# Performance work log

Hardware: AMD Instinct MI355X
Metric: run time of the kernel (lower is better)

## Reference

```python
import jax, jax.numpy as jnp
import numpy as np

HIDDEN = 4096
N_HEADS = 32
N_KV_HEADS = 8
HEAD_DIM = HIDDEN // N_HEADS  # 128
ROPE_THETA = 10000.0


def rotate_half(x):
    x1, x2 = jnp.split(x, 2, axis=-1)
    return jnp.concatenate((-x2, x1), axis=-1)


def rope_cos_sin(seq_len, dim, theta, dtype):
    inv_freq = 1.0 / (theta ** (jnp.arange(0, dim, 2, dtype=jnp.float32) / dim))
    t = jnp.arange(seq_len, dtype=jnp.float32)
    freqs = jnp.outer(t, inv_freq)               # [S, D/2]
    emb = jnp.concatenate((freqs, freqs), axis=-1)  # [S, D]
    return jnp.cos(emb).astype(dtype), jnp.sin(emb).astype(dtype)


def setup_inputs() -> dict:
    key = jax.random.key(0)
    k0, k1, k2, k3, k4 = jax.random.split(key, 5)
    B, S = 1, 2048
    std = 1.0 / np.sqrt(HIDDEN)
    return {
        "hidden_states": jax.random.normal(k0, (B, S, HIDDEN), dtype=jnp.float32),
        "wq": jax.random.normal(k1, (N_HEADS * HEAD_DIM, HIDDEN), dtype=jnp.float32) * std,
        "wk": jax.random.normal(k2, (N_KV_HEADS * HEAD_DIM, HIDDEN), dtype=jnp.float32) * std,
        "wv": jax.random.normal(k3, (N_KV_HEADS * HEAD_DIM, HIDDEN), dtype=jnp.float32) * std,
        "wo": jax.random.normal(k4, (HIDDEN, N_HEADS * HEAD_DIM), dtype=jnp.float32) * std,
    }


def reference(hidden_states, wq, wk, wv, wo):
    B, S, _ = hidden_states.shape
    dtype = hidden_states.dtype
    G = N_HEADS // N_KV_HEADS  # query groups per kv head

    # projections (torch Linear: x @ W.T)
    q = (hidden_states @ wq.T).reshape(B, S, N_HEADS, HEAD_DIM).transpose(0, 2, 1, 3)      # [B,H,S,D]
    k = (hidden_states @ wk.T).reshape(B, S, N_KV_HEADS, HEAD_DIM).transpose(0, 2, 1, 3)   # [B,Hkv,S,D]
    v = (hidden_states @ wv.T).reshape(B, S, N_KV_HEADS, HEAD_DIM).transpose(0, 2, 1, 3)   # [B,Hkv,S,D]

    cos, sin = rope_cos_sin(S, HEAD_DIM, ROPE_THETA, dtype)  # [S,D]
    cos = cos[None, None]  # [1,1,S,D]
    sin = sin[None, None]
    q = q * cos + rotate_half(q) * sin
    k = k * cos + rotate_half(k) * sin

    # GQA: group query heads with their kv head (equivalent to repeat_interleave on kv)
    qg = q.reshape(B, N_KV_HEADS, G, S, HEAD_DIM)
    scale = 1.0 / np.sqrt(HEAD_DIM)
    scores = jnp.einsum("bkgsd,bktd->bkgst", qg, k) * scale  # [B,Hkv,G,S,S]

    causal = jnp.tril(jnp.ones((S, S), dtype=bool))
    scores = jnp.where(causal, scores, -jnp.inf)
    probs = jax.nn.softmax(scores.astype(jnp.float32), axis=-1).astype(dtype)

    out = jnp.einsum("bkgst,bktd->bkgsd", probs, v)  # [B,Hkv,G,S,D]
    out = out.reshape(B, N_HEADS, S, HEAD_DIM).transpose(0, 2, 1, 3).reshape(B, S, N_HEADS * HEAD_DIM)
    return out @ wo.T
```

## Files before the change

kernel.cpp:

```cpp
#include <hip/hip_runtime.h>
#include <hip/hip_bf16.h>


typedef _Float16 half4_t __attribute__((ext_vector_type(4)));
typedef _Float16 half8_t __attribute__((ext_vector_type(8)));
typedef float f32x4 __attribute__((ext_vector_type(4)));

#define S_LEN 2048
#define HID 4096
#define NH 32
#define NKV 8

__device__ __forceinline__ void gload_lds16(const void* g, void* l) {
  __builtin_amdgcn_global_load_lds((const __attribute__((address_space(1))) void*)g,
                                   (__attribute__((address_space(3))) void*)l, 16, 0, 0);
}

__global__ __launch_bounds__(256) void cvt_f32_f16(const float* __restrict__ src,
                                                   _Float16* __restrict__ dst, int n4) {
  int i = blockIdx.x * 256 + threadIdx.x;
  if (i >= n4) return;
  f32x4 v = *(const f32x4*)(src + (size_t)i * 4);
  half4_t h = {(_Float16)v[0], (_Float16)v[1], (_Float16)v[2], (_Float16)v[3]};
  *(half4_t*)(dst + (size_t)i * 4) = h;
}

__global__ __launch_bounds__(256) void rope_table_kernel(float* __restrict__ cost,
                                                         float* __restrict__ sint) {
  int i = blockIdx.x * 256 + threadIdx.x;
  int d = i & 63;
  int s = i >> 6;
  float inv = exp2f(-(float)d * (13.287712379549449f / 64.0f));
  float f = (float)s * inv;
  cost[i] = cosf(f);
  sint[i] = sinf(f);
}

__global__ __launch_bounds__(256) void rope_apply_q(_Float16* __restrict__ X,
                                                    const float* __restrict__ cost,
                                                    const float* __restrict__ sint) {
  int idx = blockIdx.x * 256 + threadIdx.x;
  int g = idx & 15;
  int tmp = idx >> 4;
  int h = tmp % NH;
  int s = tmp / NH;
  int d0 = g * 4;
  size_t base = (size_t)s * HID + h * 128 + d0;
  half4_t x1 = *(half4_t*)(X + base);
  half4_t x2 = *(half4_t*)(X + base + 64);
  const float* cp = cost + s * 64 + d0;
  const float* sp = sint + s * 64 + d0;
  half4_t y1, y2;
#pragma unroll
  for (int j = 0; j < 4; ++j) {
    float c = cp[j], sn = sp[j];
    float a = (float)x1[j], b = (float)x2[j];
    y1[j] = (_Float16)(a * c - b * sn);
    y2[j] = (_Float16)(b * c + a * sn);
  }
  *(half4_t*)(X + base) = y1;
  *(half4_t*)(X + base + 64) = y2;
}

__global__ __launch_bounds__(256) void rope_k2_inplace(_Float16* __restrict__ K2,
                                                       const float* __restrict__ cost,
                                                       const float* __restrict__ sint) {
  int idx = blockIdx.x * 256 + threadIdx.x;
  int g = idx & 15;
  int tmp = idx >> 4;
  int h = tmp % NKV;
  int s = tmp / NKV;
  int d0 = g * 4;
  size_t tb = (size_t)h * (S_LEN * 128) + (size_t)(s >> 4) * 2048 + (size_t)(s & 15) * 8;
  size_t a1 = tb + (size_t)(d0 >> 3) * 128 + (d0 & 7);
  size_t a2 = a1 + 1024;
  half4_t x1 = *(half4_t*)(K2 + a1);
  half4_t x2 = *(half4_t*)(K2 + a2);
  const float* cp = cost + s * 64 + d0;
  const float* sp = sint + s * 64 + d0;
  half4_t y1, y2;
#pragma unroll
  for (int j = 0; j < 4; ++j) {
    float c = cp[j], sn = sp[j];
    float a = (float)x1[j], b = (float)x2[j];
    y1[j] = (_Float16)(a * c - b * sn);
    y2[j] = (_Float16)(b * c + a * sn);
  }
  *(half4_t*)(K2 + a1) = y1;
  *(half4_t*)(K2 + a2) = y2;
}

template <int MODE>
__global__ __launch_bounds__(256) void gemmC(const _Float16* __restrict__ A,
                                             const float* __restrict__ W0,
                                             const float* __restrict__ W1,
                                             const float* __restrict__ W2,
                                             void* __restrict__ out,
                                             _Float16* __restrict__ K2,
                                             _Float16* __restrict__ V2) {
  __shared__ __align__(16) _Float16 As[2][128 * 32];
  __shared__ __align__(16) _Float16 Bs[2][128 * 32];
  const int t = threadIdx.x, w = t >> 6, l = t & 63, lr = l & 15, lg = l >> 4;
  const int m0 = blockIdx.y * 128;
  const int bx = blockIdx.x;
  const float* Wp;
  int col0, sel;
  if (MODE == 1) {
    Wp = W0; col0 = bx * 128; sel = 0;
  } else {
    if (bx < 32)      { Wp = W0; col0 = bx * 128; sel = 0; }
    else if (bx < 40) { Wp = W1; col0 = (bx - 32) * 128; sel = 1; }
    else              { Wp = W2; col0 = (bx - 40) * 128; sel = 2; }
  }
  const int wm = (w >> 1) * 64, wn = (w & 1) * 64;
  const int srowA = l >> 2, scolA = (l & 3) * 8;
  const int srowB = t >> 2, scolB = (t & 3) * 8;
  const _Float16* ap = A + (size_t)m0 * 4096 + scolA;
  const float* bp = Wp + (size_t)col0 * 4096 + scolB;

  f32x4 acc[4][4] = {};
  f32x4 br[2][2];

#define GLOAD_A(buf_, kb_)                                            \
  _Pragma("unroll") for (int it = 0; it < 2; ++it) {                  \
    const int ci = it * 4 + w;                                        \
    const int r = ci * 16 + srowA;                                    \
    gload_lds16(ap + (size_t)r * 4096 + (kb_), &As[buf_][ci * 512]);  \
  }
#define LOAD_B(kb_)                                                   \
  _Pragma("unroll") for (int it = 0; it < 2; ++it) {                  \
    const float* p = bp + (size_t)(it * 64 + srowB) * 4096 + (kb_);   \
    br[it][0] = *(const f32x4*)p;                                     \
    br[it][1] = *(const f32x4*)(p + 4);                               \
  }
#define WRITE_B(buf_)                                                 \
  _Pragma("unroll") for (int it = 0; it < 2; ++it) {                  \
    half8_t hv;                                                       \
    _Pragma("unroll") for (int j = 0; j < 4; ++j) {                   \
      hv[j] = (_Float16)br[it][0][j];                                 \
      hv[4 + j] = (_Float16)br[it][1][j];                             \
    }                                                                 \
    *(half8_t*)&Bs[buf_][(it * 64 + srowB) * 32 + scolB] = hv;        \
  }

  LOAD_B(0)
  GLOAD_A(0, 0)
  WRITE_B(0)
  LOAD_B(32)
  __syncthreads();

  int cur = 0;
  for (int kb = 0; kb < 4096; kb += 32) {
    if (kb + 32 < 4096) {
      WRITE_B(cur ^ 1)
      GLOAD_A(cur ^ 1, kb + 32)
      if (kb + 64 < 4096) LOAD_B(kb + 64)
    }
    half8_t af[4], bf[4];
#pragma unroll
    for (int mi = 0; mi < 4; ++mi)
      af[mi] = *(const half8_t*)&As[cur][(wm + mi * 16 + lr) * 32 + lg * 8];
#pragma unroll
    for (int ni = 0; ni < 4; ++ni)
      bf[ni] = *(const half8_t*)&Bs[cur][(wn + ni * 16 + lr) * 32 + lg * 8];
#pragma unroll
    for (int mi = 0; mi < 4; ++mi)
#pragma unroll
      for (int ni = 0; ni < 4; ++ni)
        acc[mi][ni] = __builtin_amdgcn_mfma_f32_16x16x32_f16(af[mi], bf[ni], acc[mi][ni], 0, 0, 0);
    __syncthreads();
    cur ^= 1;
  }
#undef GLOAD_A
#undef LOAD_B
#undef WRITE_B

#pragma unroll
  for (int mi = 0; mi < 4; ++mi) {
#pragma unroll
    for (int ni = 0; ni < 4; ++ni) {
      const int row = m0 + wm + mi * 16 + lg * 4;
      const int col = col0 + wn + ni * 16 + lr;
      if (MODE == 1) {
#pragma unroll
        for (int i = 0; i < 4; ++i)
          ((float*)out)[(size_t)(row + i) * 4096 + col] = acc[mi][ni][i];
      } else if (sel == 0) {
#pragma unroll
        for (int i = 0; i < 4; ++i)
          ((_Float16*)out)[(size_t)(row + i) * 4096 + col] = (_Float16)acc[mi][ni][i];
      } else if (sel == 1) {
        const int h = col >> 7, d = col & 127;
        const size_t kb2 = (size_t)h * (S_LEN * 128) + (size_t)(row >> 4) * 2048 +
                           (size_t)(d >> 3) * 128 + (d & 7);
#pragma unroll
        for (int i = 0; i < 4; ++i)
          K2[kb2 + ((row + i) & 15) * 8] = (_Float16)acc[mi][ni][i];
      } else {
        half4_t o;
#pragma unroll
        for (int i = 0; i < 4; ++i) o[i] = (_Float16)acc[mi][ni][i];
        *(half4_t*)(V2 + (size_t)(col >> 7) * (S_LEN * 128) + (size_t)(row >> 4) * 2048 +
                    (size_t)(col & 127) * 16 + (row & 15)) = o;
      }
    }
  }
}

__global__ __launch_bounds__(256) void attn_kernel(const _Float16* __restrict__ Q,
                                                   const _Float16* __restrict__ K2,
                                                   const _Float16* __restrict__ V2,
                                                   _Float16* __restrict__ Op,
                                                   float* __restrict__ Md) {
  const int bid = blockIdx.x;
  const int hk = bid & 7;
  const int split = (bid >> 3) & 1;
  const int qt = 63 - (bid >> 4);
  const int w = threadIdx.x >> 6;
  const int h = hk * 4 + w;
  const int l = threadIdx.x & 63;
  const int lr = l & 15;
  const int lg = l >> 4;
  const float scale = 0.08838834764831845f;
  const float LOG2E = 1.4426950408889634f;
  const float NEG = -1.0e30f;

  const int half_steps = qt + 1;
  const int kt0 = split * half_steps;
  const int kt1 = kt0 + half_steps;

  int sq[2];
  half8_t qf[2][4];
#pragma unroll
  for (int qc = 0; qc < 2; ++qc) {
    sq[qc] = qt * 32 + qc * 16 + lr;
#pragma unroll
    for (int c = 0; c < 4; ++c)
      qf[qc][c] = *(const half8_t*)(Q + (size_t)sq[qc] * HID + h * 128 + c * 32 + lg * 8);
  }
  const _Float16* Kb = K2 + (size_t)hk * (S_LEN * 128);
  const _Float16* Vb = V2 + (size_t)hk * (S_LEN * 128);

  f32x4 acc[8][2] = {};
  float m[2] = {NEG, NEG};
  float den[2] = {0.f, 0.f};

  for (int kt = kt0; kt < kt1; ++kt) {
    half8_t kf[4];
#pragma unroll
    for (int c = 0; c < 4; ++c)
      kf[c] = *(const half8_t*)(Kb + (size_t)kt * 2048 + (c * 4 + lg) * 128 + lr * 8);
    f32x4 s0 = {0.f, 0.f, 0.f, 0.f}, s1 = {0.f, 0.f, 0.f, 0.f};
#pragma unroll
    for (int c = 0; c < 4; ++c) {
      s0 = __builtin_amdgcn_mfma_f32_16x16x32_f16(kf[c], qf[0][c], s0, 0, 0, 0);
      s1 = __builtin_amdgcn_mfma_f32_16x16x32_f16(kf[c], qf[1][c], s1, 0, 0, 0);
    }
    const int kbase = kt * 16 + lg * 4;
    float sc[2][4];
#pragma unroll
    for (int i = 0; i < 4; ++i) {
      sc[0][i] = s0[i] * scale;
      sc[1][i] = s1[i] * scale;
    }
    if (kt >= 2 * qt) {
#pragma unroll
      for (int qc = 0; qc < 2; ++qc)
#pragma unroll
        for (int i = 0; i < 4; ++i)
          if (kbase + i > sq[qc]) sc[qc][i] = NEG;
    }
    half4_t pf[2];
#pragma unroll
    for (int qc = 0; qc < 2; ++qc) {
      float mx = fmaxf(fmaxf(sc[qc][0], sc[qc][1]), fmaxf(sc[qc][2], sc[qc][3]));
      mx = fmaxf(mx, __shfl_xor(mx, 16));
      mx = fmaxf(mx, __shfl_xor(mx, 32));
      if (!__all(mx - m[qc] <= 8.0f)) {
        float mn = fmaxf(m[qc], mx);
        float corr = exp2f((m[qc] - mn) * LOG2E);
        den[qc] *= corr;
#pragma unroll
        for (int dc = 0; dc < 8; ++dc)
#pragma unroll
          for (int i = 0; i < 4; ++i) acc[dc][qc][i] *= corr;
        m[qc] = mn;
      }
      float ps = 0.f, p[4];
#pragma unroll
      for (int i = 0; i < 4; ++i) {
        p[i] = exp2f((sc[qc][i] - m[qc]) * LOG2E);
        ps += p[i];
      }
      ps += __shfl_xor(ps, 16);
      ps += __shfl_xor(ps, 32);
      den[qc] += ps;
      pf[qc] = (half4_t){(_Float16)p[0], (_Float16)p[1], (_Float16)p[2], (_Float16)p[3]};
    }
#pragma unroll
    for (int dc = 0; dc < 8; ++dc) {
      half4_t vf = *(const half4_t*)(Vb + (size_t)kt * 2048 + (dc * 16 + lr) * 16 + lg * 4);
      acc[dc][0] = __builtin_amdgcn_mfma_f32_16x16x16f16(vf, pf[0], acc[dc][0], 0, 0, 0);
      acc[dc][1] = __builtin_amdgcn_mfma_f32_16x16x16f16(vf, pf[1], acc[dc][1], 0, 0, 0);
    }
  }

  _Float16* Os = Op + (size_t)split * S_LEN * HID;
#pragma unroll
  for (int qc = 0; qc < 2; ++qc) {
    float inv = den[qc] > 0.f ? 1.0f / den[qc] : 0.f;
#pragma unroll
    for (int dc = 0; dc < 8; ++dc) {
      half4_t o;
#pragma unroll
      for (int i = 0; i < 4; ++i) o[i] = (_Float16)(acc[dc][qc][i] * inv);
      *(half4_t*)(Os + (size_t)sq[qc] * HID + h * 128 + dc * 16 + lg * 4) = o;
    }
    if (lg == 0) {
      int mdix = ((split * S_LEN + sq[qc]) * NH + h) * 2;
      Md[mdix] = m[qc];
      Md[mdix + 1] = den[qc];
    }
  }
}

__global__ __launch_bounds__(256) void attn_combine(const _Float16* __restrict__ Op,
                                                    const float* __restrict__ Md,
                                                    _Float16* __restrict__ O) {
  const float LOG2E = 1.4426950408889634f;
  int idx = blockIdx.x * 256 + threadIdx.x;
  int dd = (idx & 15) * 8;
  int h = (idx >> 4) & 31;
  int s = idx >> 9;
  int base = (s * NH + h) * 2;
  float m0 = Md[base], den0 = Md[base + 1];
  float m1 = Md[S_LEN * NH * 2 + base], den1 = Md[S_LEN * NH * 2 + base + 1];
  float M = fmaxf(m0, m1);
  float w0 = den0 * exp2f((m0 - M) * LOG2E);
  float w1 = den1 * exp2f((m1 - M) * LOG2E);
  float r = 1.0f / (w0 + w1);
  w0 *= r;
  w1 *= r;
  size_t off = (size_t)s * HID + h * 128 + dd;
  half8_t a = *(const half8_t*)(Op + off);
  half8_t b = *(const half8_t*)(Op + (size_t)S_LEN * HID + off);
  half8_t o;
#pragma unroll
  for (int j = 0; j < 8; ++j) o[j] = (_Float16)(w0 * (float)a[j] + w1 * (float)b[j]);
  *(half8_t*)(O + off) = o;
}

extern "C" void kernel_launch(void* const* d_in, const int* in_sizes, int n_in,
                              void* d_out, int out_size, void* d_ws, size_t ws_size,
                              hipStream_t stream) {
  (void)in_sizes; (void)n_in; (void)out_size; (void)ws_size;
  const float* hs = (const float*)d_in[0];
  const float* wq = (const float*)d_in[1];
  const float* wk = (const float*)d_in[2];
  const float* wv = (const float*)d_in[3];
  const float* wo = (const float*)d_in[4];

  char* ws = (char*)d_ws;
  _Float16* hs_h = (_Float16*)(ws);
  _Float16* q_h  = (_Float16*)(ws + (16u << 20));
  _Float16* K2   = (_Float16*)(ws + (32u << 20));
  _Float16* V2   = (_Float16*)(ws + (36u << 20));
  float* cost    = (float*)(ws + (40u << 20));
  float* sint    = (float*)(ws + (40u << 20) + (512u << 10));
  _Float16* Op   = (_Float16*)(ws + (41u << 20));
  float* Md      = (float*)(ws + (73u << 20));
  _Float16* o_h  = hs_h;

  cvt_f32_f16<<<8192, 256, 0, stream>>>(hs, hs_h, (S_LEN * HID) / 4);
  rope_table_kernel<<<(S_LEN * 64) / 256, 256, 0, stream>>>(cost, sint);

  gemmC<0><<<dim3(48, 16), 256, 0, stream>>>(hs_h, wq, wk, wv, q_h, K2, V2);

  rope_apply_q<<<(S_LEN * NH * 16) / 256, 256, 0, stream>>>(q_h, cost, sint);
  rope_k2_inplace<<<(S_LEN * NKV * 16) / 256, 256, 0, stream>>>(K2, cost, sint);

  attn_kernel<<<1024, 256, 0, stream>>>(q_h, K2, V2, Op, Md);
  attn_combine<<<4096, 256, 0, stream>>>(Op, Md, o_h);

  gemmC<1><<<dim3(32, 16), 256, 0, stream>>>(o_h, wo, nullptr, nullptr, d_out, nullptr, nullptr);
}
```

Baseline: 393.7 us.

## Split-K the Q and output projection GEMMs into two halves with fp16 partial reduction

```diff
diff --git a/kernel.cpp b/kernel.cpp
--- a/kernel.cpp
+++ b/kernel.cpp
@@ -36,9 +36,10 @@
   sint[i] = sinf(f);
 }
 
-__global__ __launch_bounds__(256) void rope_apply_q(_Float16* __restrict__ X,
-                                                    const float* __restrict__ cost,
-                                                    const float* __restrict__ sint) {
+__global__ __launch_bounds__(256) void rope_q_comb(const _Float16* __restrict__ Qp,
+                                                   const float* __restrict__ cost,
+                                                   const float* __restrict__ sint,
+                                                   _Float16* __restrict__ q) {
   int idx = blockIdx.x * 256 + threadIdx.x;
   int g = idx & 15;
   int tmp = idx >> 4;
@@ -46,20 +47,24 @@
   int s = tmp / NH;
   int d0 = g * 4;
   size_t base = (size_t)s * HID + h * 128 + d0;
-  half4_t x1 = *(half4_t*)(X + base);
-  half4_t x2 = *(half4_t*)(X + base + 64);
+  const _Float16* Qp1 = Qp + (size_t)S_LEN * HID;
+  half4_t a1 = *(const half4_t*)(Qp + base);
+  half4_t a2 = *(const half4_t*)(Qp + base + 64);
+  half4_t b1 = *(const half4_t*)(Qp1 + base);
+  half4_t b2 = *(const half4_t*)(Qp1 + base + 64);
   const float* cp = cost + s * 64 + d0;
   const float* sp = sint + s * 64 + d0;
   half4_t y1, y2;
 #pragma unroll
   for (int j = 0; j < 4; ++j) {
     float c = cp[j], sn = sp[j];
-    float a = (float)x1[j], b = (float)x2[j];
-    y1[j] = (_Float16)(a * c - b * sn);
-    y2[j] = (_Float16)(b * c + a * sn);
-  }
-  *(half4_t*)(X + base) = y1;
-  *(half4_t*)(X + base + 64) = y2;
+    float x1 = (float)a1[j] + (float)b1[j];
+    float x2 = (float)a2[j] + (float)b2[j];
+    y1[j] = (_Float16)(x1 * c - x2 * sn);
+    y2[j] = (_Float16)(x2 * c + x1 * sn);
+  }
+  *(half4_t*)(q + base) = y1;
+  *(half4_t*)(q + base + 64) = y2;
 }
 
 __global__ __launch_bounds__(256) void rope_k2_inplace(_Float16* __restrict__ K2,
@@ -90,6 +95,22 @@
   *(half4_t*)(K2 + a2) = y2;
 }
 
+__global__ __launch_bounds__(256) void addP(const _Float16* __restrict__ P,
+                                            float* __restrict__ out) {
+  int idx = blockIdx.x * 256 + threadIdx.x;
+  size_t e = (size_t)idx * 8;
+  half8_t a = *(const half8_t*)(P + e);
+  half8_t b = *(const half8_t*)(P + (size_t)S_LEN * HID + e);
+  f32x4 r0, r1;
+#pragma unroll
+  for (int j = 0; j < 4; ++j) {
+    r0[j] = (float)a[j] + (float)b[j];
+    r1[j] = (float)a[4 + j] + (float)b[4 + j];
+  }
+  *(f32x4*)(out + e) = r0;
+  *(f32x4*)(out + e + 4) = r1;
+}
+
 template <int MODE>
 __global__ __launch_bounds__(256) void gemmC(const _Float16* __restrict__ A,
                                              const float* __restrict__ W0,
@@ -98,20 +119,20 @@
                                              void* __restrict__ out,
                                              _Float16* __restrict__ K2,
                                              _Float16* __restrict__ V2) {
+  const int bx = blockIdx.x, z = blockIdx.z;
+  const float* Wp;
+  int col0, sel, kb0, KN;
+  if (MODE == 0) {
+    if (bx < 32)      { Wp = W0; col0 = bx * 128; sel = 0; kb0 = z * 2048; KN = 2048; }
+    else if (bx < 40) { if (z) return; Wp = W1; col0 = (bx - 32) * 128; sel = 1; kb0 = 0; KN = 4096; }
+    else              { if (z) return; Wp = W2; col0 = (bx - 40) * 128; sel = 2; kb0 = 0; KN = 4096; }
+  } else {
+    Wp = W0; col0 = bx * 128; sel = 0; kb0 = z * 2048; KN = 2048;
+  }
   __shared__ __align__(16) _Float16 As[2][128 * 32];
   __shared__ __align__(16) _Float16 Bs[2][128 * 32];
   const int t = threadIdx.x, w = t >> 6, l = t & 63, lr = l & 15, lg = l >> 4;
   const int m0 = blockIdx.y * 128;
-  const int bx = blockIdx.x;
-  const float* Wp;
-  int col0, sel;
-  if (MODE == 1) {
-    Wp = W0; col0 = bx * 128; sel = 0;
-  } else {
-    if (bx < 32)      { Wp = W0; col0 = bx * 128; sel = 0; }
-    else if (bx < 40) { Wp = W1; col0 = (bx - 32) * 128; sel = 1; }
-    else              { Wp = W2; col0 = (bx - 40) * 128; sel = 2; }
-  }
   const int wm = (w >> 1) * 64, wn = (w & 1) * 64;
   const int srowA = l >> 2, scolA = (l & 3) * 8;
   const int srowB = t >> 2, scolB = (t & 3) * 8;
@@ -143,18 +164,19 @@
     *(half8_t*)&Bs[buf_][(it * 64 + srowB) * 32 + scolB] = hv;        \
   }
 
-  LOAD_B(0)
-  GLOAD_A(0, 0)
+  const int kend = kb0 + KN;
+  LOAD_B(kb0)
+  GLOAD_A(0, kb0)
   WRITE_B(0)
-  LOAD_B(32)
+  LOAD_B(kb0 + 32)
   __syncthreads();
 
   int cur = 0;
-  for (int kb = 0; kb < 4096; kb += 32) {
-    if (kb + 32 < 4096) {
+  for (int kb = kb0; kb < kend; kb += 32) {
+    if (kb + 32 < kend) {
       WRITE_B(cur ^ 1)
       GLOAD_A(cur ^ 1, kb + 32)
-      if (kb + 64 < 4096) LOAD_B(kb + 64)
+      if (kb + 64 < kend) LOAD_B(kb + 64)
     }
     half8_t af[4], bf[4];
 #pragma unroll
@@ -181,14 +203,11 @@
     for (int ni = 0; ni < 4; ++ni) {
       const int row = m0 + wm + mi * 16 + lg * 4;
       const int col = col0 + wn + ni * 16 + lr;
-      if (MODE == 1) {
+      if (sel == 0) {
+        _Float16* o = (_Float16*)out + (size_t)z * S_LEN * HID;
 #pragma unroll
         for (int i = 0; i < 4; ++i)
-          ((float*)out)[(size_t)(row + i) * 4096 + col] = acc[mi][ni][i];
-      } else if (sel == 0) {
-#pragma unroll
-        for (int i = 0; i < 4; ++i)
-          ((_Float16*)out)[(size_t)(row + i) * 4096 + col] = (_Float16)acc[mi][ni][i];
+          o[(size_t)(row + i) * 4096 + col] = (_Float16)acc[mi][ni][i];
       } else if (sel == 1) {
         const int h = col >> 7, d = col & 127;
         const size_t kb2 = (size_t)h * (S_LEN * 128) + (size_t)(row >> 4) * 2048 +
@@ -367,20 +386,21 @@
   _Float16* V2   = (_Float16*)(ws + (36u << 20));
   float* cost    = (float*)(ws + (40u << 20));
   float* sint    = (float*)(ws + (40u << 20) + (512u << 10));
-  _Float16* Op   = (_Float16*)(ws + (41u << 20));
+  _Float16* Pbuf = (_Float16*)(ws + (41u << 20));
   float* Md      = (float*)(ws + (73u << 20));
   _Float16* o_h  = hs_h;
 
   cvt_f32_f16<<<8192, 256, 0, stream>>>(hs, hs_h, (S_LEN * HID) / 4);
   rope_table_kernel<<<(S_LEN * 64) / 256, 256, 0, stream>>>(cost, sint);
 
-  gemmC<0><<<dim3(48, 16), 256, 0, stream>>>(hs_h, wq, wk, wv, q_h, K2, V2);
-
-  rope_apply_q<<<(S_LEN * NH * 16) / 256, 256, 0, stream>>>(q_h, cost, sint);
+  gemmC<0><<<dim3(48, 16, 2), 256, 0, stream>>>(hs_h, wq, wk, wv, Pbuf, K2, V2);
+
+  rope_q_comb<<<4096, 256, 0, stream>>>(Pbuf, cost, sint, q_h);
   rope_k2_inplace<<<(S_LEN * NKV * 16) / 256, 256, 0, stream>>>(K2, cost, sint);
 
-  attn_kernel<<<1024, 256, 0, stream>>>(q_h, K2, V2, Op, Md);
-  attn_combine<<<4096, 256, 0, stream>>>(Op, Md, o_h);
-
-  gemmC<1><<<dim3(32, 16), 256, 0, stream>>>(o_h, wo, nullptr, nullptr, d_out, nullptr, nullptr);
-}
+  attn_kernel<<<1024, 256, 0, stream>>>(q_h, K2, V2, Pbuf, Md);
+  attn_combine<<<4096, 256, 0, stream>>>(Pbuf, Md, o_h);
+
+  gemmC<2><<<dim3(32, 16, 2), 256, 0, stream>>>(o_h, wo, nullptr, nullptr, Pbuf, nullptr, nullptr);
+  addP<<<4096, 256, 0, stream>>>(Pbuf, (float*)d_out);
+}
```

New measurement: 412.8 us. 1.05x slower.

## Pre-convert weights to fp16 and use triple-buffered async LDS GEMM pipeline

Applied to the files above, without the earlier changes.

```diff
diff --git a/kernel.cpp b/kernel.cpp
--- a/kernel.cpp
+++ b/kernel.cpp
@@ -23,6 +23,23 @@
   f32x4 v = *(const f32x4*)(src + (size_t)i * 4);
   half4_t h = {(_Float16)v[0], (_Float16)v[1], (_Float16)v[2], (_Float16)v[3]};
   *(half4_t*)(dst + (size_t)i * 4) = h;
+}
+
+__global__ __launch_bounds__(256) void cvt_qkv(const float* __restrict__ wq,
+                                               const float* __restrict__ wk,
+                                               const float* __restrict__ wv,
+                                               _Float16* __restrict__ dst, int n4) {
+  int i = blockIdx.x * 256 + threadIdx.x;
+  if (i >= n4) return;
+  size_t e = (size_t)i * 4;
+  const float* src;
+  size_t off;
+  if (e < (size_t)4096 * 4096)      { src = wq; off = e; }
+  else if (e < (size_t)5120 * 4096) { src = wk; off = e - (size_t)4096 * 4096; }
+  else                              { src = wv; off = e - (size_t)5120 * 4096; }
+  f32x4 v = *(const f32x4*)(src + off);
+  half4_t h = {(_Float16)v[0], (_Float16)v[1], (_Float16)v[2], (_Float16)v[3]};
+  *(half4_t*)(dst + e) = h;
 }
 
 __global__ __launch_bounds__(256) void rope_table_kernel(float* __restrict__ cost,
@@ -91,89 +108,64 @@
 }
 
 template <int MODE>
-__global__ __launch_bounds__(256) void gemmC(const _Float16* __restrict__ A,
-                                             const float* __restrict__ W0,
-                                             const float* __restrict__ W1,
-                                             const float* __restrict__ W2,
+__global__ __launch_bounds__(256) void gemmT(const _Float16* __restrict__ A,
+                                             const _Float16* __restrict__ W,
                                              void* __restrict__ out,
                                              _Float16* __restrict__ K2,
                                              _Float16* __restrict__ V2) {
-  __shared__ __align__(16) _Float16 As[2][128 * 32];
-  __shared__ __align__(16) _Float16 Bs[2][128 * 32];
+  const int id = blockIdx.x;
+  const int xcd = id & 7, slot = id >> 3;
+  const int c = (MODE == 0) ? (xcd * 6 + (slot >> 4)) : (xcd * 4 + (slot >> 4));
+  const int m0 = (slot & 15) * 128;
+  const int col0 = c * 128;
+  __shared__ __align__(16) _Float16 As[3][128 * 32];
+  __shared__ __align__(16) _Float16 Bs[3][128 * 32];
   const int t = threadIdx.x, w = t >> 6, l = t & 63, lr = l & 15, lg = l >> 4;
-  const int m0 = blockIdx.y * 128;
-  const int bx = blockIdx.x;
-  const float* Wp;
-  int col0, sel;
-  if (MODE == 1) {
-    Wp = W0; col0 = bx * 128; sel = 0;
-  } else {
-    if (bx < 32)      { Wp = W0; col0 = bx * 128; sel = 0; }
-    else if (bx < 40) { Wp = W1; col0 = (bx - 32) * 128; sel = 1; }
-    else              { Wp = W2; col0 = (bx - 40) * 128; sel = 2; }
-  }
   const int wm = (w >> 1) * 64, wn = (w & 1) * 64;
-  const int srowA = l >> 2, scolA = (l & 3) * 8;
-  const int srowB = t >> 2, scolB = (t & 3) * 8;
-  const _Float16* ap = A + (size_t)m0 * 4096 + scolA;
-  const float* bp = Wp + (size_t)col0 * 4096 + scolB;
+  const int srow = l >> 2, scol = (l & 3) * 8;
+  const _Float16* ap = A + (size_t)m0 * 4096 + scol;
+  const _Float16* bp = W + (size_t)col0 * 4096 + scol;
 
   f32x4 acc[4][4] = {};
-  f32x4 br[2][2];
-
-#define GLOAD_A(buf_, kb_)                                            \
+
+#define STAGE(buf_, kb_)                                              \
   _Pragma("unroll") for (int it = 0; it < 2; ++it) {                  \
     const int ci = it * 4 + w;                                        \
-    const int r = ci * 16 + srowA;                                    \
+    const int r = ci * 16 + srow;                                     \
     gload_lds16(ap + (size_t)r * 4096 + (kb_), &As[buf_][ci * 512]);  \
-  }
-#define LOAD_B(kb_)                                                   \
-  _Pragma("unroll") for (int it = 0; it < 2; ++it) {                  \
-    const float* p = bp + (size_t)(it * 64 + srowB) * 4096 + (kb_);   \
-    br[it][0] = *(const f32x4*)p;                                     \
-    br[it][1] = *(const f32x4*)(p + 4);                               \
-  }
-#define WRITE_B(buf_)                                                 \
-  _Pragma("unroll") for (int it = 0; it < 2; ++it) {                  \
-    half8_t hv;                                                       \
-    _Pragma("unroll") for (int j = 0; j < 4; ++j) {                   \
-      hv[j] = (_Float16)br[it][0][j];                                 \
-      hv[4 + j] = (_Float16)br[it][1][j];                             \
-    }                                                                 \
-    *(half8_t*)&Bs[buf_][(it * 64 + srowB) * 32 + scolB] = hv;        \
-  }
-
-  LOAD_B(0)
-  GLOAD_A(0, 0)
-  WRITE_B(0)
-  LOAD_B(32)
-  __syncthreads();
-
-  int cur = 0;
-  for (int kb = 0; kb < 4096; kb += 32) {
-    if (kb + 32 < 4096) {
-      WRITE_B(cur ^ 1)
-      GLOAD_A(cur ^ 1, kb + 32)
-      if (kb + 64 < 4096) LOAD_B(kb + 64)
-    }
+    gload_lds16(bp + (size_t)r * 4096 + (kb_), &Bs[buf_][ci * 512]);  \
+  }
+
+  STAGE(0, 0)
+  STAGE(1, 32)
+
+  for (int k = 0; k < 128; ++k) {
+    const int kb2 = (k + 2) * 32;
+    const int buf = k % 3;
+    __builtin_amdgcn_s_barrier();
+    __builtin_amdgcn_sched_barrier(0);
+    if (kb2 < 4096) {
+      STAGE((k + 2) % 3, kb2)
+      asm volatile("s_waitcnt vmcnt(4)" ::: "memory");
+    } else {
+      asm volatile("s_waitcnt vmcnt(0)" ::: "memory");
+    }
+    __builtin_amdgcn_sched_barrier(0);
+    __builtin_amdgcn_s_barrier();
     half8_t af[4], bf[4];
 #pragma unroll
     for (int mi = 0; mi < 4; ++mi)
-      af[mi] = *(const half8_t*)&As[cur][(wm + mi * 16 + lr) * 32 + lg * 8];
+      af[mi] = *(const half8_t*)&As[buf][(wm + mi * 16 + lr) * 32 + lg * 8];
 #pragma unroll
     for (int ni = 0; ni < 4; ++ni)
-      bf[ni] = *(const half8_t*)&Bs[cur][(wn + ni * 16 + lr) * 32 + lg * 8];
+      bf[ni] = *(const half8_t*)&Bs[buf][(wn + ni * 16 + lr) * 32 + lg * 8];
 #pragma unroll
     for (int mi = 0; mi < 4; ++mi)
 #pragma unroll
       for (int ni = 0; ni < 4; ++ni)
         acc[mi][ni] = __builtin_amdgcn_mfma_f32_16x16x32_f16(af[mi], bf[ni], acc[mi][ni], 0, 0, 0);
-    __syncthreads();
-    cur ^= 1;
-  }
-#undef GLOAD_A
-#undef LOAD_B
-#undef WRITE_B
+  }
+#undef STAGE
 
 #pragma unroll
   for (int mi = 0; mi < 4; ++mi) {
@@ -185,23 +177,27 @@
 #pragma unroll
         for (int i = 0; i < 4; ++i)
           ((float*)out)[(size_t)(row + i) * 4096 + col] = acc[mi][ni][i];
-      } else if (sel == 0) {
-#pragma unroll
-        for (int i = 0; i < 4; ++i)
-          ((_Float16*)out)[(size_t)(row + i) * 4096 + col] = (_Float16)acc[mi][ni][i];
-      } else if (sel == 1) {
-        const int h = col >> 7, d = col & 127;
-        const size_t kb2 = (size_t)h * (S_LEN * 128) + (size_t)(row >> 4) * 2048 +
-                           (size_t)(d >> 3) * 128 + (d & 7);
-#pragma unroll
-        for (int i = 0; i < 4; ++i)
-          K2[kb2 + ((row + i) & 15) * 8] = (_Float16)acc[mi][ni][i];
       } else {
-        half4_t o;
-#pragma unroll
-        for (int i = 0; i < 4; ++i) o[i] = (_Float16)acc[mi][ni][i];
-        *(half4_t*)(V2 + (size_t)(col >> 7) * (S_LEN * 128) + (size_t)(row >> 4) * 2048 +
-                    (size_t)(col & 127) * 16 + (row & 15)) = o;
+        if (col < 4096) {
+#pragma unroll
+          for (int i = 0; i < 4; ++i)
+            ((_Float16*)out)[(size_t)(row + i) * 4096 + col] = (_Float16)acc[mi][ni][i];
+        } else if (col < 5120) {
+          const int cl = col - 4096;
+          const int h = cl >> 7, d = cl & 127;
+          const size_t kk = (size_t)h * (S_LEN * 128) + (size_t)(row >> 4) * 2048 +
+                            (size_t)(d >> 3) * 128 + (d & 7);
+#pragma unroll
+          for (int i = 0; i < 4; ++i)
+            K2[kk + ((row + i) & 15) * 8] = (_Float16)acc[mi][ni][i];
+        } else {
+          const int cl = col - 5120;
+          half4_t o;
+#pragma unroll
+          for (int i = 0; i < 4; ++i) o[i] = (_Float16)acc[mi][ni][i];
+          *(half4_t*)(V2 + (size_t)(cl >> 7) * (S_LEN * 128) + (size_t)(row >> 4) * 2048 +
+                      (size_t)(cl & 127) * 16 + (row & 15)) = o;
+        }
       }
     }
   }
@@ -367,14 +363,17 @@
   _Float16* V2   = (_Float16*)(ws + (36u << 20));
   float* cost    = (float*)(ws + (40u << 20));
   float* sint    = (float*)(ws + (40u << 20) + (512u << 10));
-  _Float16* Op   = (_Float16*)(ws + (41u << 20));
+  _Float16* wqkv = (_Float16*)(ws + (41u << 20));
+  _Float16* Op   = wqkv;
   float* Md      = (float*)(ws + (73u << 20));
+  _Float16* wo_h = wqkv;
   _Float16* o_h  = hs_h;
 
   cvt_f32_f16<<<8192, 256, 0, stream>>>(hs, hs_h, (S_LEN * HID) / 4);
   rope_table_kernel<<<(S_LEN * 64) / 256, 256, 0, stream>>>(cost, sint);
-
-  gemmC<0><<<dim3(48, 16), 256, 0, stream>>>(hs_h, wq, wk, wv, q_h, K2, V2);
+  cvt_qkv<<<24576, 256, 0, stream>>>(wq, wk, wv, wqkv, (6144 * 4096) / 4);
+
+  gemmT<0><<<768, 256, 0, stream>>>(hs_h, wqkv, q_h, K2, V2);
 
   rope_apply_q<<<(S_LEN * NH * 16) / 256, 256, 0, stream>>>(q_h, cost, sint);
   rope_k2_inplace<<<(S_LEN * NKV * 16) / 256, 256, 0, stream>>>(K2, cost, sint);
@@ -382,5 +381,6 @@
   attn_kernel<<<1024, 256, 0, stream>>>(q_h, K2, V2, Op, Md);
   attn_combine<<<4096, 256, 0, stream>>>(Op, Md, o_h);
 
-  gemmC<1><<<dim3(32, 16), 256, 0, stream>>>(o_h, wo, nullptr, nullptr, d_out, nullptr, nullptr);
-}
+  cvt_f32_f16<<<16384, 256, 0, stream>>>(wo, wo_h, (HID * HID) / 4);
+  gemmT<1><<<512, 256, 0, stream>>>(o_h, wo_h, d_out, nullptr, nullptr);
+}
```

Result: no change. 388.5 us (-1.3%).
